# Performance work log

Hardware: AMD Instinct MI355X
Metric: run time of the kernel (lower is better)

Reference implementation:

```python
import jax, jax.numpy as jnp
import numpy as np

ANCHOR_PX = (32, 64, 96, 128)
FIELD = 16.0
POOL, TILES = 2, 3
TAU, NMS_IOU = 0.5, 0.3
MAX_DET = 512
HF, WF, DF = 128, 128, 512
HIDDEN = 1024


def _create_anchors():
    # anchors centered on the field grid, rows ordered (i, j, k): x,y = upper-left, w=h=size
    ii, jj, kk = np.meshgrid(np.arange(HF), np.arange(WF), np.arange(len(ANCHOR_PX)), indexing='ij')
    sz = np.asarray(ANCHOR_PX, np.float32)[kk]
    x = jj * FIELD + FIELD / 2 - sz / 2
    y = ii * FIELD + FIELD / 2 - sz / 2
    return np.stack([x.ravel(), y.ravel(), sz.ravel(), sz.ravel()], axis=1).astype(np.float32)


def setup_inputs() -> dict:
    key = jax.random.key(0)
    ks = jax.random.split(key, 8)
    return {
        'features': jax.random.normal(ks[0], (HF, WF, DF), jnp.float32),
        'rpn_obj': jax.random.normal(ks[1], (HF, WF, 2 * len(ANCHOR_PX)), jnp.float32),
        'rpn_reg': 0.1 * jax.random.normal(ks[2], (HF, WF, 4 * len(ANCHOR_PX)), jnp.float32),
        'anchors': jnp.asarray(_create_anchors()),
        'W1': 0.02 * jax.random.normal(ks[3], (TILES * TILES * DF, HIDDEN), jnp.float32),
        'b1': jnp.zeros((HIDDEN,), jnp.float32),
        'W2': 0.02 * jax.random.normal(ks[4], (HIDDEN, HIDDEN), jnp.float32),
        'b2': jnp.zeros((HIDDEN,), jnp.float32),
        'W3': 0.02 * jax.random.normal(ks[5], (HIDDEN, 4), jnp.float32),
        'b3': jnp.zeros((4,), jnp.float32),
    }


def _map_outputs(output, anchors):
    # faithful port of map_outputs: 3D RPN tensor -> per-anchor rows via gather
    K = len(ANCHOR_PX)
    ap = jnp.asarray(ANCHOR_PX, jnp.float32)
    idx = jnp.argmax(anchors[:, 3:4] == ap[None, :], axis=1).astype(jnp.int32)
    px = ((anchors[:, 0] + anchors[:, 2] / 2) / FIELD).astype(jnp.int32)
    py = ((anchors[:, 1] + anchors[:, 3] / 2) / FIELD).astype(jnp.int32)
    H, W, D = output.shape
    reshaped = output.reshape(H, W, K, D // K)
    return reshaped[py, px, idx]  # (Na, D//K)


def _unparameterize(reg, anchors):
    acx = anchors[:, 0] + anchors[:, 2] / 2
    acy = anchors[:, 1] + anchors[:, 3] / 2
    cx = acx + reg[:, 0] * anchors[:, 2]
    cy = acy + reg[:, 1] * anchors[:, 3]
    w = anchors[:, 2] * jnp.exp(reg[:, 2])
    h = anchors[:, 3] * jnp.exp(reg[:, 3])
    return jnp.stack([cx - w / 2, cy - h / 2, w, h], axis=1)


def _iou_matrix(boxes):
    x1, y1 = boxes[:, 0], boxes[:, 1]
    x2, y2 = x1 + boxes[:, 2], y1 + boxes[:, 3]
    ix = jnp.maximum(0.0, jnp.minimum(x2[:, None], x2[None, :]) - jnp.maximum(x1[:, None], x1[None, :]))
    iy = jnp.maximum(0.0, jnp.minimum(y2[:, None], y2[None, :]) - jnp.maximum(y1[:, None], y1[None, :]))
    inter = ix * iy
    area = boxes[:, 2] * boxes[:, 3]
    return inter / (area[:, None] + area[None, :] - inter + 1e-8)


def _nms_keep(iou, valid, thr):
    # greedy NMS on score-sorted boxes: sequential scan over rows
    n = valid.shape[0]
    rng = jnp.arange(n)
    def step(keep, i):
        suppressed = jnp.any((iou[i] > thr) & keep & (rng < i))
        k = valid[i] & jnp.logical_not(suppressed)
        return keep.at[i].set(k), k
    keep, _ = jax.lax.scan(step, jnp.zeros((n,), bool), rng)
    return keep


def _roialign(features, boxes):
    # pool x pool bilinear samples per tile, tiles x tiles tiles per box, max-pooled per tile
    M = boxes.shape[0]
    T = TILES * POOL
    t = (jnp.arange(T, dtype=jnp.float32) + 0.5) / T
    fx = (boxes[:, 0:1] + t[None, :] * boxes[:, 2:3]) / FIELD - 0.5  # (M, T)
    fy = (boxes[:, 1:2] + t[None, :] * boxes[:, 3:4]) / FIELD - 0.5
    def grid(c, n):
        c = jnp.clip(c, 0.0, n - 1.0)
        c0 = jnp.floor(c).astype(jnp.int32)
        c1 = jnp.minimum(c0 + 1, n - 1)
        return c0, c1, c - c0
    x0, x1, wx = grid(fx, WF)
    y0, y1, wy = grid(fy, HF)
    def g(yi, xi):
        return features[yi[:, :, None], xi[:, None, :]]  # (M, T, T, D)
    wy0, wy1 = (1 - wy)[:, :, None, None], wy[:, :, None, None]
    wx0, wx1 = (1 - wx)[:, None, :, None], wx[:, None, :, None]
    val = g(y0, x0) * wy0 * wx0 + g(y0, x1) * wy0 * wx1 + g(y1, x0) * wy1 * wx0 + g(y1, x1) * wy1 * wx1
    val = val.reshape(M, TILES, POOL, TILES, POOL, DF)
    return jnp.max(val, axis=(2, 4))  # (M, TILES, TILES, D)


def reference(features, rpn_obj, rpn_reg, anchors, W1, b1, W2, b2, W3, b3):
    obj = _map_outputs(rpn_obj, anchors)            # (Na, 2)
    reg = _map_outputs(rpn_reg, anchors)            # (Na, 4)
    scores = jax.nn.softmax(obj, axis=1)[:, 1]      # objectness
    boxes = _unparameterize(reg, anchors)           # proposals (Na, 4)
    # threshold + top-k (fixed-shape surrogate for boolean_mask)
    masked = jnp.where(scores > TAU, scores, -jnp.inf)
    top_scores, top_idx = jax.lax.top_k(masked, MAX_DET)
    valid = jnp.isfinite(top_scores)
    sel = boxes[top_idx]                            # (MAX_DET, 4)
    keep = _nms_keep(_iou_matrix(sel), valid, NMS_IOU)
    # roialign + fast-rcnn refinement head
    pooled = _roialign(features, sel).reshape(MAX_DET, -1)
    h = jax.nn.relu(pooled @ W1 + b1)
    h = jax.nn.relu(h @ W2 + b2)
    deltas = h @ W3 + b3
    refined = _unparameterize(deltas, sel)
    sc = jnp.where(valid, top_scores, 0.0)
    out = jnp.concatenate([refined, sc[:, None]], axis=1)
    return out * keep[:, None].astype(out.dtype)    # (MAX_DET, 5)
```

## Files before the change

### kernel.cpp

```cpp
#include <hip/hip_runtime.h>
#include <math.h>

#define HFD 128
#define WFD 128
#define DFD 512
#define KA  4
#define NA  (HFD*WFD*KA)
#define MAXD 512
#define HID 1024
#define FIN 4608
#define CMAX 2048
#define NBUCK 1025
#define BINCAP 64
#define TAUF 0.5f
#define NMS_THR 0.3f
#define SPLITK 4

typedef __bf16 bf16x8 __attribute__((ext_vector_type(8)));
typedef float  floatx4 __attribute__((ext_vector_type(4)));

__device__ __forceinline__ unsigned short f2bf(float x) {
    unsigned u = __float_as_uint(x);
    unsigned r = (u + 0x7FFFu + ((u >> 16) & 1u)) >> 16;
    return (unsigned short)r;
}

__global__ __launch_bounds__(256)
void front_kernel(const float* __restrict__ rpn_obj,
                  unsigned* __restrict__ hist,
                  unsigned long long* __restrict__ bins,
                  const float* __restrict__ W1,
                  unsigned short* __restrict__ W1t,
                  const float* __restrict__ W2,
                  unsigned short* __restrict__ W2t) {
    __shared__ float tile[32][33];
    int b = blockIdx.x;
    if (b < 256) {
        int n = b * 256 + threadIdx.x;
        float2 o = ((const float2*)rpn_obj)[n];
        float m  = fmaxf(o.x, o.y);
        float e0 = expf(o.x - m), e1 = expf(o.y - m);
        float s  = e1 / (e0 + e1);
        if (s > TAUF) {
            unsigned bits = __float_as_uint(s);
            unsigned bk = (bits - 0x3F000000u) >> 13;
            unsigned slot = atomicAdd(&hist[bk], 1u);
            if (slot < BINCAP)
                bins[bk * BINCAP + slot] =
                    ((unsigned long long)bits << 32) |
                    (unsigned long long)(~(unsigned)n);
        }
        return;
    }
    b -= 256;
    const float* W; unsigned short* Wt; int K, N;
    if (b < (FIN / 32) * (HID / 32)) { W = W1; Wt = W1t; K = FIN; N = HID; }
    else { b -= (FIN / 32) * (HID / 32); W = W2; Wt = W2t; K = HID; N = HID; }
    int bn = (b & (N / 32 - 1)) * 32;
    int bk = (b / (N / 32)) * 32;
    int tx = threadIdx.x & 31, ty = threadIdx.x >> 5;
#pragma unroll
    for (int r = 0; r < 32; r += 8)
        tile[ty + r][tx] = W[(long)(bk + ty + r) * N + bn + tx];
    __syncthreads();
#pragma unroll
    for (int r = 0; r < 32; r += 8)
        Wt[(long)(bn + ty + r) * K + bk + tx] = f2bf(tile[tx][ty + r]);
}

__global__ __launch_bounds__(1024)
void tgs_kernel(const unsigned* __restrict__ hist,
                const unsigned long long* __restrict__ bins,
                const float* __restrict__ rpn_reg,
                const float* __restrict__ anchors,
                float* __restrict__ sel,
                float* __restrict__ top_score,
                unsigned* __restrict__ valid_g) {
    __shared__ unsigned long long keys[CMAX];
    __shared__ unsigned Hs[NBUCK];
    __shared__ unsigned Ssc[1024];
    __shared__ unsigned cntS;
    __shared__ unsigned thrS;

    int tid = threadIdx.x;
    int wave = tid >> 6, lane = tid & 63;

    if (tid == 0) cntS = 0u;
    for (int i = tid; i < NBUCK; i += 1024) Hs[i] = hist[i];
    __syncthreads();
    unsigned sv = Hs[tid + 1];
    Ssc[tid] = sv;
    __syncthreads();
    for (int d = 1; d < 1024; d <<= 1) {
        unsigned add = (tid + d < 1024) ? Ssc[tid + d] : 0u;
        __syncthreads();
        Ssc[tid] += add;
        __syncthreads();
    }
    if (tid == 0 && Ssc[0] < MAXD) thrS = 0u;
    {
        unsigned Scur = Ssc[tid];
        unsigned Snxt = (tid == 1023) ? 0u : Ssc[tid + 1];
        if (Scur >= MAXD && Snxt < MAXD) thrS = (unsigned)(tid + 1);
    }
    __syncthreads();
    unsigned thr = thrS;

    for (int b = (int)thr + wave; b < NBUCK; b += 16) {
        unsigned c = Hs[b]; if (c > BINCAP) c = BINCAP;
        unsigned base = 0;
        if (lane == 0 && c > 0) base = atomicAdd(&cntS, c);
        base = __shfl(base, 0);
        if (c > 0 && lane < c && base + lane < CMAX)
            keys[base + lane] = bins[(long)b * BINCAP + lane];
    }
    __syncthreads();
    unsigned cnt = cntS; if (cnt > CMAX) cnt = CMAX;
    int SN = (cnt <= 1024) ? 1024 : CMAX;
    for (int i = tid; i < SN; i += 1024)
        if (i >= (int)cnt) keys[i] = 0ULL;
    __syncthreads();

    for (int k = 2; k <= SN; k <<= 1) {
        for (int j = k >> 1; j > 0; j >>= 1) {
            for (int i = tid; i < SN; i += 1024) {
                int ixj = i ^ j;
                if (ixj > i) {
                    unsigned long long a = keys[i], b = keys[ixj];
                    bool up = ((i & k) == 0);
                    if ((a < b) == up) { keys[i] = b; keys[ixj] = a; }
                }
            }
            __syncthreads();
        }
    }

    if (tid < MAXD) {
        unsigned long long e = keys[tid];
        unsigned sbits = (unsigned)(e >> 32);
        bool v = (sbits != 0u);
        unsigned idx = v ? (unsigned)(~(unsigned)e) : 0u;
        int cell = idx >> 2, kk = idx & 3;
        float4 rg = *(const float4*)&rpn_reg[cell * 16 + 4 * kk];
        float4 an = *(const float4*)&anchors[idx * 4];
        float acx = an.x + an.z * 0.5f;
        float acy = an.y + an.w * 0.5f;
        float cx = acx + rg.x * an.z;
        float cy = acy + rg.y * an.w;
        float w  = an.z * expf(rg.z);
        float h  = an.w * expf(rg.w);
        ((float4*)sel)[tid] = make_float4(cx - 0.5f * w, cy - 0.5f * h, w, h);
        top_score[tid] = v ? __uint_as_float(sbits) : 0.0f;
        valid_g[tid]   = v ? 1u : 0u;
    }
}

__global__ __launch_bounds__(512)
void iou_mask_kernel(const float* __restrict__ sel,
                     unsigned long long* __restrict__ mask) {
    int i = blockIdx.x;
    int j = threadIdx.x;
    float4 bi = ((const float4*)sel)[i];
    float4 bj = ((const float4*)sel)[j];
    float x2i = bi.x + bi.z, y2i = bi.y + bi.w;
    float x2j = bj.x + bj.z, y2j = bj.y + bj.w;
    float ai = bi.z * bi.w, aj = bj.z * bj.w;
    float ix = fmaxf(0.0f, fminf(x2i, x2j) - fmaxf(bi.x, bj.x));
    float iy = fmaxf(0.0f, fminf(y2i, y2j) - fmaxf(bi.y, bj.y));
    float inter = ix * iy;
    float iou = inter / (ai + aj - inter + 1e-8f);
    unsigned long long bal = __ballot(iou > NMS_THR);
    if ((j & 63) == 0) mask[i * 8 + (j >> 6)] = bal;
}

__global__ __launch_bounds__(64)
void nms_scan_kernel(const unsigned long long* __restrict__ mask,
                     const unsigned* __restrict__ valid,
                     unsigned* __restrict__ keep) {
    int lane = threadIdx.x;
    unsigned long long w[8][8];
#pragma unroll
    for (int g = 0; g < 8; ++g)
#pragma unroll
        for (int t = 0; t < 8; ++t)
            if (t <= g) w[g][t] = mask[(g * 64 + lane) * 8 + t];
    unsigned long long vb[8];
#pragma unroll
    for (int g = 0; g < 8; ++g)
        vb[g] = __ballot(valid[g * 64 + lane] != 0u);

    unsigned long long keepw[8];
#pragma unroll
    for (int g = 0; g < 8; ++g) {
        bool pre = false;
#pragma unroll
        for (int t = 0; t < 8; ++t)
            if (t < g) pre = pre || ((w[g][t] & keepw[t]) != 0ULL);
        unsigned long long alive = vb[g] & ~__ballot(pre);
        unsigned long long intra = w[g][g];
        unsigned long long kg = 0ULL;
#pragma unroll
        for (int b = 0; b < 64; ++b) {
            unsigned long long sup = __ballot((intra >> b) & 1ULL);
            if ((alive >> b) & 1ULL) {
                kg |= 1ULL << b;
                alive &= ~sup;
            }
        }
        keepw[g] = kg;
        keep[g * 64 + lane] = (unsigned)((kg >> lane) & 1ULL);
    }
}

__global__ __launch_bounds__(256)
void roialign_kernel(const float* __restrict__ feat,
                     const float* __restrict__ sel,
                     unsigned short* __restrict__ pooled) {
    int blk = blockIdx.x;
    int mrow = blk / 9;
    int tile = blk - mrow * 9;
    int tp = tile / 3, tq = tile - tp * 3;
    int c = threadIdx.x;
    float4 b = ((const float4*)sel)[mrow];
    float vmax0 = -INFINITY, vmax1 = -INFINITY;
#pragma unroll
    for (int dp = 0; dp < 2; ++dp) {
        int p = tp * 2 + dp;
        float fy = (b.y + ((float)p + 0.5f) / 6.0f * b.w) / 16.0f - 0.5f;
        fy = fminf(fmaxf(fy, 0.0f), 127.0f);
        int y0 = (int)floorf(fy);
        int y1 = min(y0 + 1, 127);
        float wy = fy - (float)y0;
#pragma unroll
        for (int dq = 0; dq < 2; ++dq) {
            int q = tq * 2 + dq;
            float fx = (b.x + ((float)q + 0.5f) / 6.0f * b.z) / 16.0f - 0.5f;
            fx = fminf(fmaxf(fx, 0.0f), 127.0f);
            int x0 = (int)floorf(fx);
            int x1 = min(x0 + 1, 127);
            float wx = fx - (float)x0;
            const float* f00 = feat + (y0 * WFD + x0) * DFD;
            const float* f01 = feat + (y0 * WFD + x1) * DFD;
            const float* f10 = feat + (y1 * WFD + x0) * DFD;
            const float* f11 = feat + (y1 * WFD + x1) * DFD;
            float w00 = (1.0f - wy) * (1.0f - wx);
            float w01 = (1.0f - wy) * wx;
            float w10 = wy * (1.0f - wx);
            float w11 = wy * wx;
            float v0 = f00[c] * w00 + f01[c] * w01 + f10[c] * w10 + f11[c] * w11;
            float v1 = f00[c + 256] * w00 + f01[c + 256] * w01 +
                       f10[c + 256] * w10 + f11[c + 256] * w11;
            vmax0 = fmaxf(vmax0, v0);
            vmax1 = fmaxf(vmax1, v1);
        }
    }
    pooled[mrow * FIN + tile * DFD + c] = f2bf(vmax0);
    pooled[mrow * FIN + tile * DFD + c + 256] = f2bf(vmax1);
}

#define LDK 72
__global__ __launch_bounds__(256)
void mfma_gemm_kernel(const unsigned short* __restrict__ A,
                      const unsigned short* __restrict__ Bt,
                      float* __restrict__ Cpart,
                      int M, int N, int K) {
    __shared__ unsigned short As[64 * LDK];
    __shared__ unsigned short Bs[64 * LDK];
    int tid = threadIdx.x;
    int wave = tid >> 6, lane = tid & 63;
    int bm = blockIdx.y * 64, bn = blockIdx.x * 64;
    int KC = K / SPLITK;
    int ks = blockIdx.z * KC;

    floatx4 acc[4] = {};
    int lr = tid >> 2;
    int lk = (tid & 3) << 4;
    int frow = lane & 15, quad = lane >> 4;

    const unsigned short* Ap = A + (long)(bm + lr) * K + lk;
    const unsigned short* Bp = Bt + (long)(bn + lr) * K + lk;

    for (int k0 = ks; k0 < ks + KC; k0 += 64) {
        uint4 a0 = *(const uint4*)(Ap + k0);
        uint4 a1 = *(const uint4*)(Ap + k0 + 8);
        uint4 b0 = *(const uint4*)(Bp + k0);
        uint4 b1 = *(const uint4*)(Bp + k0 + 8);
        *(uint4*)&As[lr * LDK + lk] = a0;
        *(uint4*)&As[lr * LDK + lk + 8] = a1;
        *(uint4*)&Bs[lr * LDK + lk] = b0;
        *(uint4*)&Bs[lr * LDK + lk + 8] = b1;
        __syncthreads();
        bf16x8 af0 = *(const bf16x8*)&As[(wave * 16 + frow) * LDK + quad * 8];
        bf16x8 af1 = *(const bf16x8*)&As[(wave * 16 + frow) * LDK + 32 + quad * 8];
#pragma unroll
        for (int t = 0; t < 4; ++t) {
            bf16x8 b0v = *(const bf16x8*)&Bs[(t * 16 + frow) * LDK + quad * 8];
            bf16x8 b1v = *(const bf16x8*)&Bs[(t * 16 + frow) * LDK + 32 + quad * 8];
            acc[t] = __builtin_amdgcn_mfma_f32_16x16x32_bf16(af0, b0v, acc[t], 0, 0, 0);
            acc[t] = __builtin_amdgcn_mfma_f32_16x16x32_bf16(af1, b1v, acc[t], 0, 0, 0);
        }
        __syncthreads();
    }

    float* Cp = Cpart + (long)blockIdx.z * M * N;
#pragma unroll
    for (int t = 0; t < 4; ++t) {
#pragma unroll
        for (int r = 0; r < 4; ++r) {
            int m = bm + wave * 16 + quad * 4 + r;
            int n = bn + t * 16 + frow;
            Cp[(long)m * N + n] = acc[t][r];
        }
    }
}

__global__ __launch_bounds__(256)
void reduce_bias_relu_kernel(const float* __restrict__ Cpart,
                             const float* __restrict__ bias,
                             unsigned short* __restrict__ out_bf,
                             int MN, int N) {
    int i4 = (blockIdx.x * blockDim.x + threadIdx.x) * 4;
    if (i4 >= MN) return;
    float4 s = *(const float4*)&Cpart[i4];
#pragma unroll
    for (int z = 1; z < SPLITK; ++z) {
        float4 p = *(const float4*)&Cpart[(long)z * MN + i4];
        s.x += p.x; s.y += p.y; s.z += p.z; s.w += p.w;
    }
    int n = i4 & (N - 1);
    float4 bi = *(const float4*)&bias[n];
    s.x = fmaxf(s.x + bi.x, 0.0f);
    s.y = fmaxf(s.y + bi.y, 0.0f);
    s.z = fmaxf(s.z + bi.z, 0.0f);
    s.w = fmaxf(s.w + bi.w, 0.0f);
    uint2 o;
    o.x = (unsigned)f2bf(s.x) | ((unsigned)f2bf(s.y) << 16);
    o.y = (unsigned)f2bf(s.z) | ((unsigned)f2bf(s.w) << 16);
    *(uint2*)&out_bf[i4] = o;
}

__global__ __launch_bounds__(256)
void rowhead_kernel(const float* __restrict__ Cpart,
                    const float* __restrict__ b2,
                    const float* __restrict__ W3,
                    const float* __restrict__ b3,
                    const float* __restrict__ sel,
                    const float* __restrict__ top_score,
                    const unsigned* __restrict__ valid,
                    const unsigned* __restrict__ keep,
                    float* __restrict__ out) {
    __shared__ float red[4][4];
    int r = blockIdx.x, t = threadIdx.x;
    int wave = t >> 6, lane = t & 63;
    int c = t * 4;
    const int MN = MAXD * HID;
    float4 s = *(const float4*)&Cpart[(long)r * HID + c];
#pragma unroll
    for (int z = 1; z < SPLITK; ++z) {
        float4 p = *(const float4*)&Cpart[(long)z * MN + (long)r * HID + c];
        s.x += p.x; s.y += p.y; s.z += p.z; s.w += p.w;
    }
    float4 bi = *(const float4*)&b2[c];
    float h[4];
    h[0] = fmaxf(s.x + bi.x, 0.0f);
    h[1] = fmaxf(s.y + bi.y, 0.0f);
    h[2] = fmaxf(s.z + bi.z, 0.0f);
    h[3] = fmaxf(s.w + bi.w, 0.0f);
    float a0 = 0.f, a1 = 0.f, a2 = 0.f, a3 = 0.f;
#pragma unroll
    for (int i = 0; i < 4; ++i) {
        float4 w = *(const float4*)&W3[(c + i) * 4];
        a0 += h[i] * w.x; a1 += h[i] * w.y;
        a2 += h[i] * w.z; a3 += h[i] * w.w;
    }
#pragma unroll
    for (int off = 32; off > 0; off >>= 1) {
        a0 += __shfl_down(a0, off);
        a1 += __shfl_down(a1, off);
        a2 += __shfl_down(a2, off);
        a3 += __shfl_down(a3, off);
    }
    if (lane == 0) {
        red[wave][0] = a0; red[wave][1] = a1;
        red[wave][2] = a2; red[wave][3] = a3;
    }
    __syncthreads();
    if (t == 0) {
        float d0 = red[0][0] + red[1][0] + red[2][0] + red[3][0] + b3[0];
        float d1 = red[0][1] + red[1][1] + red[2][1] + red[3][1] + b3[1];
        float d2 = red[0][2] + red[1][2] + red[2][2] + red[3][2] + b3[2];
        float d3 = red[0][3] + red[1][3] + red[2][3] + red[3][3] + b3[3];
        if (keep[r] != 0u) {
            float4 b = ((const float4*)sel)[r];
            float acx = b.x + 0.5f * b.z;
            float acy = b.y + 0.5f * b.w;
            float cx = acx + d0 * b.z;
            float cy = acy + d1 * b.w;
            float nw = b.z * expf(d2);
            float nh = b.w * expf(d3);
            out[r * 5 + 0] = cx - 0.5f * nw;
            out[r * 5 + 1] = cy - 0.5f * nh;
            out[r * 5 + 2] = nw;
            out[r * 5 + 3] = nh;
            out[r * 5 + 4] = (valid[r] != 0u) ? top_score[r] : 0.0f;
        } else {
            out[r * 5 + 0] = 0.0f;
            out[r * 5 + 1] = 0.0f;
            out[r * 5 + 2] = 0.0f;
            out[r * 5 + 3] = 0.0f;
            out[r * 5 + 4] = 0.0f;
        }
    }
}

extern "C" void kernel_launch(void* const* d_in, const int* in_sizes, int n_in,
                              void* d_out, int out_size, void* d_ws, size_t ws_size,
                              hipStream_t stream) {
    const float* features = (const float*)d_in[0];
    const float* rpn_obj  = (const float*)d_in[1];
    const float* rpn_reg  = (const float*)d_in[2];
    const float* anchors  = (const float*)d_in[3];
    const float* W1 = (const float*)d_in[4];
    const float* b1 = (const float*)d_in[5];
    const float* W2 = (const float*)d_in[6];
    const float* b2 = (const float*)d_in[7];
    const float* W3 = (const float*)d_in[8];
    const float* b3 = (const float*)d_in[9];
    float* out = (float*)d_out;

    char* ws = (char*)d_ws;
    size_t off = 0;
    auto alloc = [&](size_t bytes) {
        char* p = ws + off;
        off += (bytes + 255) & ~(size_t)255;
        return p;
    };
    unsigned* hist      = (unsigned*)alloc(NBUCK * sizeof(unsigned));
    unsigned long long* bins =
        (unsigned long long*)alloc((size_t)NBUCK * BINCAP * 8);
    float*    sel       = (float*)alloc(MAXD * 4 * sizeof(float));
    float*    top_score = (float*)alloc(MAXD * sizeof(float));
    unsigned* valid     = (unsigned*)alloc(MAXD * sizeof(unsigned));
    unsigned* keep      = (unsigned*)alloc(MAXD * sizeof(unsigned));
    unsigned long long* mask = (unsigned long long*)alloc(MAXD * 8 * 8);
    unsigned short* pooled = (unsigned short*)alloc((size_t)MAXD * FIN * 2);
    unsigned short* W1t = (unsigned short*)alloc((size_t)FIN * HID * 2);
    unsigned short* W2t = (unsigned short*)alloc((size_t)HID * HID * 2);
    unsigned short* h1  = (unsigned short*)alloc((size_t)MAXD * HID * 2);
    float*    Cpart     = (float*)alloc((size_t)SPLITK * MAXD * HID * sizeof(float));
    (void)ws_size; (void)in_sizes; (void)n_in; (void)out_size;

    const int TBLOCKS = (FIN / 32) * (HID / 32) + (HID / 32) * (HID / 32);
    hipMemsetAsync(hist, 0, NBUCK * sizeof(unsigned), stream);
    front_kernel<<<256 + TBLOCKS, 256, 0, stream>>>(rpn_obj, hist, bins,
                                                    W1, W1t, W2, W2t);
    tgs_kernel<<<1, 1024, 0, stream>>>(hist, bins, rpn_reg, anchors,
                                       sel, top_score, valid);
    iou_mask_kernel<<<MAXD, 512, 0, stream>>>(sel, mask);
    nms_scan_kernel<<<1, 64, 0, stream>>>(mask, valid, keep);
    roialign_kernel<<<MAXD * 9, 256, 0, stream>>>(features, sel, pooled);

    const int MN = MAXD * HID;
    mfma_gemm_kernel<<<dim3(HID / 64, MAXD / 64, SPLITK), 256, 0, stream>>>(
        pooled, W1t, Cpart, MAXD, HID, FIN);
    reduce_bias_relu_kernel<<<MN / 4 / 256, 256, 0, stream>>>(
        Cpart, b1, h1, MN, HID);
    mfma_gemm_kernel<<<dim3(HID / 64, MAXD / 64, SPLITK), 256, 0, stream>>>(
        h1, W2t, Cpart, MAXD, HID, HID);
    rowhead_kernel<<<MAXD, 256, 0, stream>>>(Cpart, b2, W3, b3, sel,
                                             top_score, valid, keep, out);
}
```

Baseline: 195.6 us.

## Restructure NMS scan to propagate suppression forward per kept box column

Rewrites the single-wave NMS scan so each kept box immediately marks suppression for all later boxes through a per-lane 8-bit suppression word, instead of holding the lower-triangular mask block in registers and doing cross-group AND tests. Mask columns are streamed in one group at a time with prefetch of the next column. This is meant to cut register pressure (the old kernel held up to 36 64-bit words per lane) and the serial cross-group checks. The trade-off is a ballot plus an 8-way bit gather on every one of the 512 serial iterations, and the inner loop is no longer unrolled.

```diff
diff --git a/kernel.cpp b/kernel.cpp
--- a/kernel.cpp
+++ b/kernel.cpp
@@ -173,42 +173,46 @@
     if ((j & 63) == 0) mask[i * 8 + (j >> 6)] = bal;
 }
 
-__global__ __launch_bounds__(64)
+__global__ __launch_bounds__(64, 1)
 void nms_scan_kernel(const unsigned long long* __restrict__ mask,
                      const unsigned* __restrict__ valid,
                      unsigned* __restrict__ keep) {
     int lane = threadIdx.x;
-    unsigned long long w[8][8];
-#pragma unroll
-    for (int g = 0; g < 8; ++g)
-#pragma unroll
-        for (int t = 0; t < 8; ++t)
-            if (t <= g) w[g][t] = mask[(g * 64 + lane) * 8 + t];
     unsigned long long vb[8];
 #pragma unroll
     for (int g = 0; g < 8; ++g)
         vb[g] = __ballot(valid[g * 64 + lane] != 0u);
 
-    unsigned long long keepw[8];
-#pragma unroll
-    for (int g = 0; g < 8; ++g) {
-        bool pre = false;
-#pragma unroll
-        for (int t = 0; t < 8; ++t)
-            if (t < g) pre = pre || ((w[g][t] & keepw[t]) != 0ULL);
-        unsigned long long alive = vb[g] & ~__ballot(pre);
-        unsigned long long intra = w[g][g];
+    unsigned long long cw[8], cwn[8];
+#pragma unroll
+    for (int g = 0; g < 8; ++g)
+        cw[g] = mask[(g * 64 + lane) * 8 + 0];
+
+    unsigned supp8 = 0u;
+#pragma unroll
+    for (int G = 0; G < 8; ++G) {
+        if (G < 7) {
+#pragma unroll
+            for (int g = 0; g < 8; ++g)
+                cwn[g] = mask[(g * 64 + lane) * 8 + (G + 1)];
+        }
         unsigned long long kg = 0ULL;
-#pragma unroll
+        unsigned long long vbG = vb[G];
         for (int b = 0; b < 64; ++b) {
-            unsigned long long sup = __ballot((intra >> b) & 1ULL);
-            if ((alive >> b) & 1ULL) {
-                kg |= 1ULL << b;
-                alive &= ~sup;
+            unsigned long long sg = __ballot((supp8 >> G) & 1u);
+            unsigned long long bi = 1ULL << b;
+            if (((vbG & bi) != 0ULL) && ((sg & bi) == 0ULL)) {
+                kg |= bi;
+                unsigned nb = 0u;
+#pragma unroll
+                for (int g = 0; g < 8; ++g)
+                    nb |= (unsigned)((cw[g] >> b) & 1ULL) << g;
+                supp8 |= nb;
             }
         }
-        keepw[g] = kg;
-        keep[g * 64 + lane] = (unsigned)((kg >> lane) & 1ULL);
+        keep[G * 64 + lane] = (unsigned)((kg >> lane) & 1ULL);
+#pragma unroll
+        for (int g = 0; g < 8; ++g) cw[g] = cwn[g];
     }
 }
 
```

After: 216.8 us. +10.8%, slower.
